# Performance work log

Hardware: AMD Instinct MI355X
Metric: run time of the kernel (lower is better)

Reference implementation:

```python
import jax, jax.numpy as jnp
import numpy as np

N_SLICES = 2  # init kwarg n_slices


def affine_grid_3d(theta, D, H, W):
    """torch.nn.functional.affine_grid for 5D output, align_corners=False.
    theta: [B,3,4]; returns grid [B,D,H,W,3] with last dim (x,y,z) ~ (W,H,D)."""
    xs = (jnp.arange(W, dtype=theta.dtype) + 0.5) * (2.0 / W) - 1.0
    ys = (jnp.arange(H, dtype=theta.dtype) + 0.5) * (2.0 / H) - 1.0
    zs = (jnp.arange(D, dtype=theta.dtype) + 0.5) * (2.0 / D) - 1.0
    zz, yy, xx = jnp.meshgrid(zs, ys, xs, indexing='ij')
    base = jnp.stack([xx, yy, zz, jnp.ones_like(xx)], axis=-1)  # [D,H,W,4]
    return jnp.einsum('bij,dhwj->bdhwi', theta, base)  # [B,D,H,W,3]


def grid_sample_3d_zeros(vol, grid):
    """torch.nn.functional.grid_sample, mode='bilinear' (trilinear for 5D),
    padding_mode='zeros', align_corners=False.
    vol: [B,C,D,H,W]; grid: [B,D,H,W,3] normalized xyz coords."""
    B, C, D, H, W = vol.shape
    ix = ((grid[..., 0] + 1.0) * W - 1.0) * 0.5
    iy = ((grid[..., 1] + 1.0) * H - 1.0) * 0.5
    iz = ((grid[..., 2] + 1.0) * D - 1.0) * 0.5
    ix0 = jnp.floor(ix); iy0 = jnp.floor(iy); iz0 = jnp.floor(iz)
    fx = ix - ix0; fy = iy - iy0; fz = iz - iz0

    def gather(v, z, y, x):  # v: [C,D,H,W], idx: [D,H,W] -> [C,D,H,W]
        return v[:, z, y, x]

    out = jnp.zeros((B, C, D, H, W), vol.dtype)
    for dz in (0, 1):
        for dy in (0, 1):
            for dx in (0, 1):
                xi = ix0 + dx; yi = iy0 + dy; zi = iz0 + dz
                w = (jnp.where(dx, fx, 1.0 - fx)
                     * jnp.where(dy, fy, 1.0 - fy)
                     * jnp.where(dz, fz, 1.0 - fz))
                valid = ((xi >= 0) & (xi < W) & (yi >= 0) & (yi < H)
                         & (zi >= 0) & (zi < D))
                xc = jnp.clip(xi, 0, W - 1).astype(jnp.int32)
                yc = jnp.clip(yi, 0, H - 1).astype(jnp.int32)
                zc = jnp.clip(zi, 0, D - 1).astype(jnp.int32)
                vals = jax.vmap(gather)(vol, zc, yc, xc)  # [B,C,D,H,W]
                out = out + vals * (w * valid)[:, None]
    return out


def skip_connector(x, b_grid_affines):
    B, C, SPAT, _ = x.shape
    # zero volume with the 2D slice stack placed at the central W-plane
    vol = jnp.zeros((B, C, SPAT, SPAT, SPAT), x.dtype).at[..., SPAT // 2].set(x)
    chunks = jnp.split(vol, N_SLICES, axis=1)
    outs = []
    for i in range(N_SLICES):
        aff = b_grid_affines[i].astype(jnp.float32)  # [B,4,4]
        # get_zooms: column norms of rotation block
        zooms = jnp.sqrt((aff[:, :3, :3] ** 2).sum(axis=1))  # [B,3]
        # rescale_rot_components_with_diag(aff, 1/zooms) == aff @ diag(1/zx,1/zy,1/zz,1)
        scale = jnp.concatenate([1.0 / zooms, jnp.ones((aff.shape[0], 1), aff.dtype)], axis=1)
        aff = aff * scale[:, None, :]
        theta = jnp.linalg.inv(aff)[:, :3, :]  # [B,3,4]
        grid = affine_grid_3d(theta, SPAT, SPAT, SPAT)
        outs.append(grid_sample_3d_zeros(chunks[i], grid))
    return jnp.concatenate(outs, axis=1)  # [B,C,SPAT,SPAT,SPAT]


def setup_inputs() -> dict:
    key = jax.random.key(0)
    k1, k2 = jax.random.split(key)
    B, C, SPAT = 2, 32, 96
    x = jax.random.normal(k1, (B, C, SPAT, SPAT), dtype=jnp.float32)
    # near-identity invertible homogeneous affines for the two views (SA, HLA)
    noise = 0.1 * jax.random.normal(k2, (2, B, 4, 4), dtype=jnp.float32)
    aff = jnp.eye(4, dtype=jnp.float32)[None, None] + noise
    aff = aff.at[..., 3, :].set(jnp.array([0.0, 0.0, 0.0, 1.0], dtype=jnp.float32))
    return {"x": x, "b_grid_affines": aff}


def reference(x, b_grid_affines):
    return skip_connector(x, b_grid_affines)
```

## Files before the change

### kernel.cpp

```cpp
#include <hip/hip_runtime.h>
#include <math.h>

#define SPAT 96
#define PLANE (SPAT*SPAT*SPAT)
#define IMG   (SPAT*SPAT)
#define OUT_FLOATS (64 * PLANE)

__device__ inline void invert4(const float m[16], float inv[16]) {
    inv[0]  =  m[5]*m[10]*m[15] - m[5]*m[11]*m[14] - m[9]*m[6]*m[15] + m[9]*m[7]*m[14] + m[13]*m[6]*m[11] - m[13]*m[7]*m[10];
    inv[4]  = -m[4]*m[10]*m[15] + m[4]*m[11]*m[14] + m[8]*m[6]*m[15] - m[8]*m[7]*m[14] - m[12]*m[6]*m[11] + m[12]*m[7]*m[10];
    inv[8]  =  m[4]*m[9]*m[15]  - m[4]*m[11]*m[13] - m[8]*m[5]*m[15] + m[8]*m[7]*m[13] + m[12]*m[5]*m[11] - m[12]*m[7]*m[9];
    inv[12] = -m[4]*m[9]*m[14]  + m[4]*m[10]*m[13] + m[8]*m[5]*m[14] - m[8]*m[6]*m[13] - m[12]*m[5]*m[10] + m[12]*m[6]*m[9];
    inv[1]  = -m[1]*m[10]*m[15] + m[1]*m[11]*m[14] + m[9]*m[2]*m[15] - m[9]*m[3]*m[14] - m[13]*m[2]*m[11] + m[13]*m[3]*m[10];
    inv[5]  =  m[0]*m[10]*m[15] - m[0]*m[11]*m[14] - m[8]*m[2]*m[15] + m[8]*m[3]*m[14] + m[12]*m[2]*m[11] - m[12]*m[3]*m[10];
    inv[9]  = -m[0]*m[9]*m[15]  + m[0]*m[11]*m[13] + m[8]*m[1]*m[15] - m[8]*m[3]*m[13] - m[12]*m[1]*m[11] + m[12]*m[3]*m[9];
    inv[13] =  m[0]*m[9]*m[14]  - m[0]*m[10]*m[13] - m[8]*m[1]*m[14] + m[8]*m[2]*m[13] + m[12]*m[1]*m[10] - m[12]*m[2]*m[9];
    inv[2]  =  m[1]*m[6]*m[15]  - m[1]*m[7]*m[14]  - m[5]*m[2]*m[15] + m[5]*m[3]*m[14] + m[13]*m[2]*m[7]  - m[13]*m[3]*m[6];
    inv[6]  = -m[0]*m[6]*m[15]  + m[0]*m[7]*m[14]  + m[4]*m[2]*m[15] - m[4]*m[3]*m[14] - m[12]*m[2]*m[7]  + m[12]*m[3]*m[6];
    inv[10] =  m[0]*m[5]*m[15]  - m[0]*m[7]*m[13]  - m[4]*m[1]*m[15] + m[4]*m[3]*m[13] + m[12]*m[1]*m[7]  - m[12]*m[3]*m[5];
    inv[14] = -m[0]*m[5]*m[14]  + m[0]*m[6]*m[13]  + m[4]*m[1]*m[14] - m[4]*m[2]*m[13] - m[12]*m[1]*m[6]  + m[12]*m[2]*m[5];
    inv[3]  = -m[1]*m[6]*m[11]  + m[1]*m[7]*m[10]  + m[5]*m[2]*m[11] - m[5]*m[3]*m[10] - m[9]*m[2]*m[7]   + m[9]*m[3]*m[6];
    inv[7]  =  m[0]*m[6]*m[11]  - m[0]*m[7]*m[10]  - m[4]*m[2]*m[11] + m[4]*m[3]*m[10] + m[8]*m[2]*m[7]   - m[8]*m[3]*m[6];
    inv[11] = -m[0]*m[5]*m[11]  + m[0]*m[7]*m[9]   + m[4]*m[1]*m[11] - m[4]*m[3]*m[9]  - m[8]*m[1]*m[7]   + m[8]*m[3]*m[5];
    inv[15] =  m[0]*m[5]*m[10]  - m[0]*m[6]*m[9]   - m[4]*m[1]*m[10] + m[4]*m[2]*m[9]  + m[8]*m[1]*m[6]   - m[8]*m[2]*m[5];
    float det  = m[0]*inv[0] + m[1]*inv[4] + m[2]*inv[8] + m[3]*inv[12];
    float rdet = 1.0f / det;
    for (int i = 0; i < 16; ++i) inv[i] *= rdet;
}

__global__ __launch_bounds__(256) void zero_kernel(float4* __restrict__ out) {
    const size_t n4 = OUT_FLOATS / 4;
    size_t i = (size_t)blockIdx.x * 256 + threadIdx.x;
    size_t stride = (size_t)gridDim.x * 256;
    float4 z = make_float4(0.f, 0.f, 0.f, 0.f);
    for (; i < n4; i += stride) out[i] = z;
}

__global__ __launch_bounds__(256) void slab_kernel(
        const float* __restrict__ xin,
        const float* __restrict__ aff_in,
        float* __restrict__ out) {
    __shared__ float Ms[12];
    int sb = blockIdx.y;
    if (threadIdx.x == 0) {
        float A[16];
        #pragma unroll
        for (int i = 0; i < 16; ++i) A[i] = aff_in[sb * 16 + i];
        #pragma unroll
        for (int j = 0; j < 3; ++j) {
            float z = sqrtf(A[0*4+j]*A[0*4+j] + A[1*4+j]*A[1*4+j] + A[2*4+j]*A[2*4+j]);
            float rz = 1.0f / z;
            #pragma unroll
            for (int i = 0; i < 4; ++i) A[i*4+j] *= rz;
        }
        float inv[16];
        invert4(A, inv);
        #pragma unroll
        for (int r = 0; r < 3; ++r) {
            float T0 = inv[r*4+0], T1 = inv[r*4+1], T2 = inv[r*4+2], T3 = inv[r*4+3];
            Ms[r*4+0] = T0;
            Ms[r*4+1] = T1;
            Ms[r*4+2] = T2;
            Ms[r*4+3] = -47.5f * (T0 + T1 + T2) + 48.0f * T3 + 47.5f;
        }
    }
    __syncthreads();

    int t  = blockIdx.x * 256 + threadIdx.x;
    int cg = t & 3;
    int hd = t >> 2;
    int h  = hd % SPAT;
    int d  = hd / SPAT;
    int s  = sb >> 1;
    int b  = sb & 1;

    float Mxw = Ms[0], Mxh = Ms[1], Mxd = Ms[2],  Mx0 = Ms[3];
    float Myw = Ms[4], Myh = Ms[5], Myd = Ms[6],  My0 = Ms[7];
    float Mzw = Ms[8], Mzh = Ms[9], Mzd = Ms[10], Mz0 = Ms[11];

    float fh = (float)h, fd = (float)d;
    float bx = Mxh * fh + Mxd * fd + Mx0;
    float by = Myh * fh + Myd * fd + My0;
    float bz = Mzh * fh + Mzd * fd + Mz0;

    int wlo, whi;
    if (fabsf(Mxw) > 1e-6f) {
        float w1 = (47.0f - bx) / Mxw;
        float w2 = (49.0f - bx) / Mxw;
        float wmin = fminf(w1, w2), wmax = fmaxf(w1, w2);
        wlo = (int)ceilf(wmin);
        whi = (int)floorf(wmax);
        wlo = max(wlo, 0);
        whi = min(whi, SPAT - 1);
    } else {
        bool in = fabsf(bx - 48.0f) < 1.0f;
        wlo = in ? 0 : 1;
        whi = in ? SPAT - 1 : 0;
    }
    if (wlo > whi) return;

    size_t cbase = (size_t)(b * 32 + s * 16 + cg * 4);
    const float* img = xin + cbase * (size_t)IMG;
    float* op = out + cbase * (size_t)PLANE + ((size_t)d * SPAT + h) * SPAT;

    for (int w = wlo; w <= whi; ++w) {
        float fw = (float)w;
        float ix = Mxw * fw + bx;
        float wx = 1.0f - fabsf(ix - 48.0f);
        if (wx <= 0.0f) continue;
        float iy = Myw * fw + by;
        float iz = Mzw * fw + bz;

        float yf = floorf(iy), zf = floorf(iz);
        float fy = iy - yf,    fz = iz - zf;
        int y0 = (int)yf, z0 = (int)zf;
        bool vy0 = (y0 >= 0)  & (y0 <  SPAT);
        bool vy1 = (y0 >= -1) & (y0 <  SPAT - 1);
        bool vz0 = (z0 >= 0)  & (z0 <  SPAT);
        bool vz1 = (z0 >= -1) & (z0 <  SPAT - 1);
        int y0c = min(max(y0, 0),     SPAT - 1);
        int y1c = min(max(y0 + 1, 0), SPAT - 1);
        int z0c = min(max(z0, 0),     SPAT - 1);
        int z1c = min(max(z0 + 1, 0), SPAT - 1);
        float wy0 = 1.0f - fy, wy1 = fy;
        float wz0 = 1.0f - fz, wz1 = fz;
        float w00 = wx * wz0 * wy0 * ((vz0 & vy0) ? 1.0f : 0.0f);
        float w01 = wx * wz0 * wy1 * ((vz0 & vy1) ? 1.0f : 0.0f);
        float w10 = wx * wz1 * wy0 * ((vz1 & vy0) ? 1.0f : 0.0f);
        float w11 = wx * wz1 * wy1 * ((vz1 & vy1) ? 1.0f : 0.0f);
        int o00 = z0c * SPAT + y0c, o01 = z0c * SPAT + y1c;
        int o10 = z1c * SPAT + y0c, o11 = z1c * SPAT + y1c;

        #pragma unroll
        for (int c = 0; c < 4; ++c) {
            const float* ic = img + (size_t)c * IMG;
            float r = w00 * ic[o00] + w01 * ic[o01]
                    + w10 * ic[o10] + w11 * ic[o11];
            op[(size_t)c * PLANE + w] = r;
        }
    }
}

extern "C" void kernel_launch(void* const* d_in, const int* in_sizes, int n_in,
                              void* d_out, int out_size, void* d_ws, size_t ws_size,
                              hipStream_t stream) {
    const float* x   = (const float*)d_in[0];
    const float* aff = (const float*)d_in[1];
    float* out = (float*)d_out;

    zero_kernel<<<4096, 256, 0, stream>>>((float4*)out);

    dim3 grid(144, 4);
    slab_kernel<<<grid, 256, 0, stream>>>(x, aff, out);
}
```

Baseline: 243.0 us.

## Vectorize slab stores to float4 quads and split W range across thread pairs

Each thread now computes four consecutive W outputs per channel and writes them as one float4 store, instead of one scalar store per W. Threads are paired by quad parity so each interleaves over alternate quads, and the grid is doubled to match. This aims to cut the number of store transactions and raise parallelism. In exchange, it computes and writes zero-weight entries inside a quad, and it slightly raises register use.

```diff
diff --git a/kernel.cpp b/kernel.cpp
--- a/kernel.cpp
+++ b/kernel.cpp
@@ -66,13 +66,14 @@
     }
     __syncthreads();
 
-    int t  = blockIdx.x * 256 + threadIdx.x;
-    int cg = t & 3;
-    int hd = t >> 2;
-    int h  = hd % SPAT;
-    int d  = hd / SPAT;
-    int s  = sb >> 1;
-    int b  = sb & 1;
+    int t    = blockIdx.x * 256 + threadIdx.x;
+    int cg   = t & 3;
+    int qpar = (t >> 2) & 1;
+    int hd   = t >> 3;
+    int h    = hd % SPAT;
+    int d    = hd / SPAT;
+    int s    = sb >> 1;
+    int b    = sb & 1;
 
     float Mxw = Ms[0], Mxh = Ms[1], Mxd = Ms[2],  Mx0 = Ms[3];
     float Myw = Ms[4], Myh = Ms[5], Myd = Ms[6],  My0 = Ms[7];
@@ -80,63 +81,74 @@
 
     float fh = (float)h, fd = (float)d;
     float bx = Mxh * fh + Mxd * fd + Mx0;
-    float by = Myh * fh + Myd * fd + My0;
-    float bz = Mzh * fh + Mzd * fd + Mz0;
 
     int wlo, whi;
     if (fabsf(Mxw) > 1e-6f) {
-        float w1 = (47.0f - bx) / Mxw;
-        float w2 = (49.0f - bx) / Mxw;
+        float rMxw = 1.0f / Mxw;
+        float w1 = (47.0f - bx) * rMxw;
+        float w2 = (49.0f - bx) * rMxw;
         float wmin = fminf(w1, w2), wmax = fmaxf(w1, w2);
-        wlo = (int)ceilf(wmin);
-        whi = (int)floorf(wmax);
-        wlo = max(wlo, 0);
-        whi = min(whi, SPAT - 1);
+        wlo = max((int)ceilf(wmin), 0);
+        whi = min((int)floorf(wmax), SPAT - 1);
     } else {
         bool in = fabsf(bx - 48.0f) < 1.0f;
         wlo = in ? 0 : 1;
         whi = in ? SPAT - 1 : 0;
     }
     if (wlo > whi) return;
+    int qlo = (wlo >> 2) + qpar, qhi = whi >> 2;
+
+    float by = Myh * fh + Myd * fd + My0;
+    float bz = Mzh * fh + Mzd * fd + Mz0;
 
     size_t cbase = (size_t)(b * 32 + s * 16 + cg * 4);
     const float* img = xin + cbase * (size_t)IMG;
     float* op = out + cbase * (size_t)PLANE + ((size_t)d * SPAT + h) * SPAT;
 
-    for (int w = wlo; w <= whi; ++w) {
-        float fw = (float)w;
-        float ix = Mxw * fw + bx;
-        float wx = 1.0f - fabsf(ix - 48.0f);
-        if (wx <= 0.0f) continue;
-        float iy = Myw * fw + by;
-        float iz = Mzw * fw + bz;
-
-        float yf = floorf(iy), zf = floorf(iz);
-        float fy = iy - yf,    fz = iz - zf;
-        int y0 = (int)yf, z0 = (int)zf;
-        bool vy0 = (y0 >= 0)  & (y0 <  SPAT);
-        bool vy1 = (y0 >= -1) & (y0 <  SPAT - 1);
-        bool vz0 = (z0 >= 0)  & (z0 <  SPAT);
-        bool vz1 = (z0 >= -1) & (z0 <  SPAT - 1);
-        int y0c = min(max(y0, 0),     SPAT - 1);
-        int y1c = min(max(y0 + 1, 0), SPAT - 1);
-        int z0c = min(max(z0, 0),     SPAT - 1);
-        int z1c = min(max(z0 + 1, 0), SPAT - 1);
-        float wy0 = 1.0f - fy, wy1 = fy;
-        float wz0 = 1.0f - fz, wz1 = fz;
-        float w00 = wx * wz0 * wy0 * ((vz0 & vy0) ? 1.0f : 0.0f);
-        float w01 = wx * wz0 * wy1 * ((vz0 & vy1) ? 1.0f : 0.0f);
-        float w10 = wx * wz1 * wy0 * ((vz1 & vy0) ? 1.0f : 0.0f);
-        float w11 = wx * wz1 * wy1 * ((vz1 & vy1) ? 1.0f : 0.0f);
-        int o00 = z0c * SPAT + y0c, o01 = z0c * SPAT + y1c;
-        int o10 = z1c * SPAT + y0c, o11 = z1c * SPAT + y1c;
-
+    for (int q = qlo; q <= qhi; q += 2) {
+        float v[4][4];
+        #pragma unroll
+        for (int j = 0; j < 4; ++j) {
+            float fw = (float)(4 * q + j);
+            float ix = Mxw * fw + bx;
+            float wx = 1.0f - fabsf(ix - 48.0f);
+            if (wx > 0.0f) {
+                float iy = Myw * fw + by;
+                float iz = Mzw * fw + bz;
+                float yf = floorf(iy), zf = floorf(iz);
+                float fy = iy - yf,    fz = iz - zf;
+                int y0 = (int)yf, z0 = (int)zf;
+                bool vy0 = (y0 >= 0)  & (y0 <  SPAT);
+                bool vy1 = (y0 >= -1) & (y0 <  SPAT - 1);
+                bool vz0 = (z0 >= 0)  & (z0 <  SPAT);
+                bool vz1 = (z0 >= -1) & (z0 <  SPAT - 1);
+                int y0c = min(max(y0, 0),     SPAT - 1);
+                int y1c = min(max(y0 + 1, 0), SPAT - 1);
+                int z0c = min(max(z0, 0),     SPAT - 1);
+                int z1c = min(max(z0 + 1, 0), SPAT - 1);
+                float wy0 = 1.0f - fy, wy1 = fy;
+                float wz0 = 1.0f - fz, wz1 = fz;
+                float w00 = wx * wz0 * wy0 * ((vz0 & vy0) ? 1.0f : 0.0f);
+                float w01 = wx * wz0 * wy1 * ((vz0 & vy1) ? 1.0f : 0.0f);
+                float w10 = wx * wz1 * wy0 * ((vz1 & vy0) ? 1.0f : 0.0f);
+                float w11 = wx * wz1 * wy1 * ((vz1 & vy1) ? 1.0f : 0.0f);
+                int o00 = z0c * SPAT + y0c, o01 = z0c * SPAT + y1c;
+                int o10 = z1c * SPAT + y0c, o11 = z1c * SPAT + y1c;
+                #pragma unroll
+                for (int c = 0; c < 4; ++c) {
+                    const float* ic = img + (size_t)c * IMG;
+                    v[c][j] = w00 * ic[o00] + w01 * ic[o01]
+                            + w10 * ic[o10] + w11 * ic[o11];
+                }
+            } else {
+                #pragma unroll
+                for (int c = 0; c < 4; ++c) v[c][j] = 0.0f;
+            }
+        }
         #pragma unroll
         for (int c = 0; c < 4; ++c) {
-            const float* ic = img + (size_t)c * IMG;
-            float r = w00 * ic[o00] + w01 * ic[o01]
-                    + w10 * ic[o10] + w11 * ic[o11];
-            op[(size_t)c * PLANE + w] = r;
+            *reinterpret_cast<float4*>(op + (size_t)c * PLANE + 4 * q) =
+                make_float4(v[c][0], v[c][1], v[c][2], v[c][3]);
         }
     }
 }
@@ -150,6 +162,6 @@
 
     zero_kernel<<<4096, 256, 0, stream>>>((float4*)out);
 
-    dim3 grid(144, 4);
+    dim3 grid(288, 4);
     slab_kernel<<<grid, 256, 0, stream>>>(x, aff, out);
 }
```

Measured after the change: 237.2 us. 2.4% less time.
